# Optimization experiments

Hardware: AMD Instinct MI355X
Metric: run time of the kernel (lower is better)

Reference implementation:

```python
import jax, jax.numpy as jnp
import numpy as np

HIDDEN = 1024
HEADS = 16
D_HEAD = HIDDEN // HEADS  # 64
N = 2048


def setup_inputs() -> dict:
    key = jax.random.key(0)
    ks = jax.random.split(key, 12)
    s = 1.0 / np.sqrt(HIDDEN)
    return {
        "q": jax.random.normal(ks[0], (N, HIDDEN), jnp.float32),
        "k": jax.random.normal(ks[1], (N, HIDDEN), jnp.float32),
        "v": jax.random.normal(ks[2], (N, HIDDEN), jnp.float32),
        "attn_bias": jax.random.normal(ks[3], (HEADS, 1, N, N), jnp.float32),
        "Wq": jax.random.normal(ks[4], (HIDDEN, HIDDEN), jnp.float32) * s,
        "bq": jax.random.normal(ks[5], (HIDDEN,), jnp.float32) * s,
        "Wk": jax.random.normal(ks[6], (HIDDEN, HIDDEN), jnp.float32) * s,
        "bk": jax.random.normal(ks[7], (HIDDEN,), jnp.float32) * s,
        "Wv": jax.random.normal(ks[8], (HIDDEN, HIDDEN), jnp.float32) * s,
        "bv": jax.random.normal(ks[9], (HIDDEN,), jnp.float32) * s,
        "Wo": jax.random.normal(ks[10], (HIDDEN, HIDDEN), jnp.float32) * s,
        "bo": jax.random.normal(ks[11], (HIDDEN,), jnp.float32) * s,
    }


def reference(q, k, v, attn_bias, Wq, bq, Wk, bk, Wv, bv, Wo, bo):
    # q,k,v: [N, hidden]; attn_bias: [H, 1, N, N]. Attention runs over the
    # node axis (dim 0 in the torch code), inner seq dim is 1 (squeezed).
    n = q.shape[0]
    scale = D_HEAD ** -0.5
    qh = (q @ Wq.T + bq).reshape(n, HEADS, D_HEAD).transpose(1, 0, 2)  # [H,N,d]
    kh = (k @ Wk.T + bk).reshape(n, HEADS, D_HEAD).transpose(1, 0, 2)  # [H,N,d]
    vh = (v @ Wv.T + bv).reshape(n, HEADS, D_HEAD).transpose(1, 0, 2)  # [H,N,d]
    scores = jnp.einsum('hnd,hmd->hnm', qh * scale, kh) + attn_bias[:, 0]  # [H,N,N]
    attn = jax.nn.softmax(scores, axis=-1)
    ctx = jnp.einsum('hnm,hmd->hnd', attn, vh)            # [H,N,d]
    ctx = ctx.transpose(1, 0, 2).reshape(n, HEADS * D_HEAD)  # [N,hidden]
    return ctx @ Wo.T + bo
```

## Files before the change

kernel.cpp:

```cpp
#include <hip/hip_runtime.h>
#include <type_traits>
#include <utility>

#define NT 2048
#define HD 1024
#define NHEAD 16
#define DHEAD 64
#define LOG2E 1.44269504f

typedef float f32x4 __attribute__((ext_vector_type(4)));
typedef __bf16 b16x8 __attribute__((ext_vector_type(8)));
typedef short s16x8 __attribute__((ext_vector_type(8)));
typedef unsigned short u16x8 __attribute__((ext_vector_type(8)));
typedef unsigned short u16x4 __attribute__((ext_vector_type(4)));

template <typename V, typename = void>
struct mfma_takes : std::false_type {};
template <typename V>
struct mfma_takes<V, std::void_t<decltype(__builtin_amdgcn_mfma_f32_16x16x32_bf16(
                         std::declval<V>(), std::declval<V>(), std::declval<f32x4>(), 0, 0, 0))>>
    : std::true_type {};

template <typename V>
__device__ __forceinline__ f32x4 mfma_impl(V a, V b, f32x4 c) {
  return __builtin_amdgcn_mfma_f32_16x16x32_bf16(a, b, c, 0, 0, 0);
}

__device__ __forceinline__ f32x4 mfma_bf16(u16x8 a, u16x8 b, f32x4 c) {
  using V = typename std::conditional<mfma_takes<b16x8>::value, b16x8, s16x8>::type;
  return mfma_impl<V>(__builtin_bit_cast(V, a), __builtin_bit_cast(V, b), c);
}

__device__ __forceinline__ unsigned short f2bf(float f) {
  unsigned int u = __builtin_bit_cast(unsigned int, f);
  return (unsigned short)((u + 0x7FFFu + ((u >> 16) & 1u)) >> 16);
}

__device__ __forceinline__ void gload16(const unsigned short* g, unsigned short* l) {
  __builtin_amdgcn_global_load_lds(
      (__attribute__((address_space(1))) void*)(void*)(g),
      (__attribute__((address_space(3))) void*)(void*)(l), 16, 0, 0);
}

__device__ __forceinline__ void barrier_pinned() {
  __builtin_amdgcn_sched_barrier(0);
  __builtin_amdgcn_s_barrier();
  __builtin_amdgcn_sched_barrier(0);
}
#define WAIT_VM6() asm volatile("s_waitcnt vmcnt(6)" ::: "memory")
#define WAIT_VM0() asm volatile("s_waitcnt vmcnt(0)" ::: "memory")
#define WAIT_LGKM0() asm volatile("s_waitcnt lgkmcnt(0)" ::: "memory")

__global__ __launch_bounds__(256) void cvt_bf16(
    const float* __restrict__ s0, const float* __restrict__ s1, const float* __restrict__ s2,
    const float* __restrict__ s3, const float* __restrict__ s4, const float* __restrict__ s5,
    const float* __restrict__ s6,
    unsigned short* __restrict__ d0, unsigned short* __restrict__ d1, unsigned short* __restrict__ d2,
    unsigned short* __restrict__ d3, unsigned short* __restrict__ d4, unsigned short* __restrict__ d5,
    unsigned short* __restrict__ d6) {
  const int seg = blockIdx.y;
  const float* s;
  unsigned short* d;
  switch (seg) {
    case 0: s = s0; d = d0; break;
    case 1: s = s1; d = d1; break;
    case 2: s = s2; d = d2; break;
    case 3: s = s3; d = d3; break;
    case 4: s = s4; d = d4; break;
    case 5: s = s5; d = d5; break;
    default: s = s6; d = d6; break;
  }
  const int n = (seg < 3) ? NT * HD : HD * HD;
  for (int i = blockIdx.x * 2048 + threadIdx.x * 8; i < n; i += gridDim.x * 2048) {
    f32x4 f0 = *reinterpret_cast<const f32x4*>(&s[i]);
    f32x4 f1 = *reinterpret_cast<const f32x4*>(&s[i + 4]);
    u16x8 o;
#pragma unroll
    for (int e = 0; e < 4; ++e) { o[e] = f2bf(f0[e]); o[e + 4] = f2bf(f1[e]); }
    *reinterpret_cast<u16x8*>(&d[i]) = o;
  }
}

__device__ __forceinline__ void gemm64x128(
    const unsigned short* __restrict__ A, const unsigned short* __restrict__ B,
    int n0, int m0,
    unsigned short* As0, unsigned short* As1,
    unsigned short* Bs0, unsigned short* Bs1, f32x4 acc[2][4]) {
  const int tid = threadIdx.x;
  const int lane = tid & 63;
  const int wr = (tid >> 6) >> 1, wc = (tid >> 6) & 1;
  const int srow = tid >> 3;
  const int scol = (((tid & 7) ^ (srow & 7)) << 3);

  auto stage = [&](int kt, unsigned short* as, unsigned short* bs) {
#pragma unroll
    for (int p = 0; p < 2; ++p)
      gload16(&A[(size_t)(n0 + p * 32 + srow) * HD + kt + scol], as + p * 2048 + tid * 8);
#pragma unroll
    for (int p = 0; p < 4; ++p)
      gload16(&B[(size_t)(m0 + p * 32 + srow) * HD + kt + scol], bs + p * 2048 + tid * 8);
  };
  auto comp = [&](const unsigned short* as, const unsigned short* bs) {
#pragma unroll
    for (int ks = 0; ks < 2; ++ks) {
      const int q = ks * 4 + (lane >> 4);
      u16x8 a[2], b[4];
#pragma unroll
      for (int i = 0; i < 2; ++i) {
        const int row = wr * 32 + i * 16 + (lane & 15);
        a[i] = *reinterpret_cast<const u16x8*>(&as[row * 64 + ((q ^ (row & 7)) << 3)]);
      }
#pragma unroll
      for (int j = 0; j < 4; ++j) {
        const int row = wc * 64 + j * 16 + (lane & 15);
        b[j] = *reinterpret_cast<const u16x8*>(&bs[row * 64 + ((q ^ (row & 7)) << 3)]);
      }
#pragma unroll
      for (int i = 0; i < 2; ++i)
#pragma unroll
        for (int j = 0; j < 4; ++j)
          acc[i][j] = mfma_bf16(a[i], b[j], acc[i][j]);
    }
  };

  stage(0, As0, Bs0);
  stage(64, As1, Bs1);
#pragma unroll 1
  for (int s = 0; s < 14; ++s) {
    WAIT_VM6();
    barrier_pinned();
    if (s & 1) comp(As1, Bs1); else comp(As0, Bs0);
    barrier_pinned();
    if (s & 1) stage((s + 2) * 64, As1, Bs1);
    else       stage((s + 2) * 64, As0, Bs0);
  }
  WAIT_VM6();
  barrier_pinned();
  comp(As0, Bs0);
  WAIT_VM0();
  barrier_pinned();
  comp(As1, Bs1);
}

__global__ __launch_bounds__(256) void proj_gemm(
    const unsigned short* __restrict__ qb, const unsigned short* __restrict__ kb,
    const unsigned short* __restrict__ vb,
    const unsigned short* __restrict__ Wqb, const unsigned short* __restrict__ Wkb,
    const unsigned short* __restrict__ Wvb,
    const float* __restrict__ bq, const float* __restrict__ bk, const float* __restrict__ bv,
    unsigned short* __restrict__ Qh, unsigned short* __restrict__ Kh,
    unsigned short* __restrict__ Vt) {
  const int L = blockIdx.x;
  const int m = L / 96;
  const int c = L % 96;
  const int z = c / 32;
  const int n = c % 32;
  const int n0 = n * 64, m0 = m * 128;

  const unsigned short* A = (z == 0) ? qb : (z == 1) ? kb : vb;
  const unsigned short* B = (z == 0) ? Wqb : (z == 1) ? Wkb : Wvb;
  const float* bias = (z == 0) ? bq : (z == 1) ? bk : bv;

  __shared__ unsigned short As0[64 * 64], As1[64 * 64];
  __shared__ unsigned short Bs0[128 * 64], Bs1[128 * 64];

  const int tid = threadIdx.x;
  const int lane = tid & 63;
  const int wr = (tid >> 6) >> 1, wc = (tid >> 6) & 1;

  f32x4 acc[2][4] = {};
  gemm64x128(A, B, n0, m0, As0, As1, Bs0, Bs1, acc);

  const int rgrp = (lane >> 4) * 4;
  const float scale = (z == 0) ? 0.125f * LOG2E : 1.0f;
#pragma unroll
  for (int i = 0; i < 2; ++i) {
    const int nb = n0 + wr * 32 + i * 16 + rgrp;
#pragma unroll
    for (int j = 0; j < 4; ++j) {
      const int mcol = m0 + wc * 64 + j * 16 + (lane & 15);
      const float bb = bias[mcol];
      if (z == 2) {
        u16x4 pk;
#pragma unroll
        for (int r = 0; r < 4; ++r) pk[r] = f2bf(acc[i][j][r] + bb);
        *reinterpret_cast<u16x4*>(&Vt[(size_t)mcol * NT + nb]) = pk;
      } else {
        unsigned short* dst = (z == 0) ? Qh : Kh;
#pragma unroll
        for (int r = 0; r < 4; ++r)
          dst[(size_t)(nb + r) * HD + mcol] = f2bf((acc[i][j][r] + bb) * scale);
      }
    }
  }
}

__global__ __launch_bounds__(256, 2) void attn_kernel(
    const unsigned short* __restrict__ Qh, const unsigned short* __restrict__ Kh,
    const unsigned short* __restrict__ Vt, const float* __restrict__ bias,
    unsigned short* __restrict__ ctx) {
  const int id = blockIdx.x;
  const int xcd = id & 7, slot = id >> 3;
  const int h = xcd * 2 + (slot >> 5);
  const int q0 = (slot & 31) * 64;
  const int tid = threadIdx.x;
  const int lane = tid & 63;
  const int wave = tid >> 6;

  __shared__ unsigned short Ks0[128 * 64], Ks1[128 * 64];
  __shared__ unsigned short Vs0[64 * 128], Vs1[64 * 128];
  __shared__ unsigned short Ps[4 * 16 * 128];

  u16x8 qf[2];
  {
    const int qrow = q0 + wave * 16 + (lane & 15);
    const int db = (lane >> 4) * 8;
    qf[0] = *reinterpret_cast<const u16x8*>(&Qh[(size_t)qrow * HD + h * DHEAD + db]);
    qf[1] = *reinterpret_cast<const u16x8*>(&Qh[(size_t)qrow * HD + h * DHEAD + 32 + db]);
  }

  f32x4 oacc[4] = {};
  float mrun[4], lrun[4];
#pragma unroll
  for (int r = 0; r < 4; ++r) { mrun[r] = -3.0e38f; lrun[r] = 0.f; }

  const float* bias_h = bias + (size_t)h * NT * NT;
  const int qlrow = q0 + wave * 16 + (lane >> 4) * 4;
  const float* bias_l = bias_h + (size_t)qlrow * NT + (lane & 15);

  const unsigned short* Kbase = Kh + h * DHEAD;
  const unsigned short* Vbase = Vt + (size_t)h * DHEAD * NT;

  const int krow = tid >> 3;
  const int kchk = tid & 7;
  const int vrow = tid >> 4;
  const int vchk = tid & 15;

  auto stage = [&](int t, unsigned short* ks, unsigned short* vs) {
    const int kt = t * 128;
#pragma unroll
    for (int p = 0; p < 4; ++p) {
      const int r = p * 32 + krow;
      gload16(&Kbase[(size_t)(kt + r) * HD + ((kchk ^ (r & 7)) << 3)], ks + p * 2048 + tid * 8);
    }
#pragma unroll
    for (int p = 0; p < 4; ++p) {
      const int r = p * 16 + vrow;
      gload16(&Vbase[(size_t)r * NT + kt + ((vchk ^ (r & 7)) << 3)], vs + p * 2048 + tid * 8);
    }
  };

  float br[8][4];
#pragma unroll
  for (int j = 0; j < 8; ++j)
#pragma unroll
    for (int r = 0; r < 4; ++r) br[j][r] = bias_l[(size_t)r * NT + j * 16];
  stage(0, Ks0, Vs0);
  WAIT_VM0();
  barrier_pinned();

  unsigned short* const psw = Ps + wave * 2048;

#pragma unroll 1
  for (int t = 0; t < NT / 128; ++t) {
    const bool more = (t + 1 < NT / 128);
    const unsigned short* ks = (t & 1) ? Ks1 : Ks0;
    const unsigned short* vs = (t & 1) ? Vs1 : Vs0;

    if (more) stage(t + 1, (t & 1) ? Ks0 : Ks1, (t & 1) ? Vs0 : Vs1);

    f32x4 s[8] = {};
#pragma unroll
    for (int kss = 0; kss < 2; ++kss) {
      const int q = kss * 4 + (lane >> 4);
#pragma unroll
      for (int j = 0; j < 8; ++j) {
        const int row = j * 16 + (lane & 15);
        u16x8 kf = *reinterpret_cast<const u16x8*>(&ks[row * 64 + ((q ^ (row & 7)) << 3)]);
        s[j] = mfma_bf16(qf[kss], kf, s[j]);
      }
    }
#pragma unroll
    for (int j = 0; j < 8; ++j)
#pragma unroll
      for (int r = 0; r < 4; ++r) s[j][r] = fmaf(br[j][r], LOG2E, s[j][r]);

    if (more) {
      const float* bp = bias_l + (size_t)(t + 1) * 128;
#pragma unroll
      for (int j = 0; j < 8; ++j)
#pragma unroll
        for (int r = 0; r < 4; ++r) br[j][r] = bp[(size_t)r * NT + j * 16];
    }

    float mnew[4];
#pragma unroll
    for (int r = 0; r < 4; ++r) {
      float mx = s[0][r];
#pragma unroll
      for (int j = 1; j < 8; ++j) mx = fmaxf(mx, s[j][r]);
      mx = fmaxf(mx, __shfl_xor(mx, 1));
      mx = fmaxf(mx, __shfl_xor(mx, 2));
      mx = fmaxf(mx, __shfl_xor(mx, 4));
      mx = fmaxf(mx, __shfl_xor(mx, 8));
      mnew[r] = fmaxf(mrun[r], mx);
    }
#pragma unroll
    for (int r = 0; r < 4; ++r) {
      const float corr = exp2f(mrun[r] - mnew[r]);
      lrun[r] *= corr;
#pragma unroll
      for (int nd = 0; nd < 4; ++nd) oacc[nd][r] *= corr;
      mrun[r] = mnew[r];
    }
    float psum[4] = {0.f, 0.f, 0.f, 0.f};
#pragma unroll
    for (int j = 0; j < 8; ++j) {
      const int chkbase = j * 2 + ((lane >> 3) & 1);
      const int cofs = lane & 7;
#pragma unroll
      for (int r = 0; r < 4; ++r) {
        const int row = (lane >> 4) * 4 + r;
        const float p = exp2f(s[j][r] - mrun[r]);
        psum[r] += p;
        psw[row * 128 + ((chkbase ^ (row & 7)) << 3) + cofs] = f2bf(p);
      }
    }
#pragma unroll
    for (int r = 0; r < 4; ++r) {
      float tsum = psum[r];
      tsum += __shfl_xor(tsum, 1);
      tsum += __shfl_xor(tsum, 2);
      tsum += __shfl_xor(tsum, 4);
      tsum += __shfl_xor(tsum, 8);
      lrun[r] += tsum;
    }

#pragma unroll
    for (int kk = 0; kk < 4; ++kk) {
      const int q = kk * 4 + (lane >> 4);
      const int prow = lane & 15;
      u16x8 pa = *reinterpret_cast<const u16x8*>(&psw[prow * 128 + ((q ^ (prow & 7)) << 3)]);
#pragma unroll
      for (int nd = 0; nd < 4; ++nd) {
        const int vr = nd * 16 + (lane & 15);
        u16x8 vb = *reinterpret_cast<const u16x8*>(&vs[vr * 128 + ((q ^ (vr & 7)) << 3)]);
        oacc[nd] = mfma_bf16(pa, vb, oacc[nd]);
      }
    }

    WAIT_VM0();
    barrier_pinned();
  }

#pragma unroll
  for (int nd = 0; nd < 4; ++nd) {
#pragma unroll
    for (int r = 0; r < 4; ++r) {
      const float val = oacc[nd][r] / lrun[r];
      ctx[(size_t)(qlrow + r) * HD + h * DHEAD + nd * 16 + (lane & 15)] = f2bf(val);
    }
  }
}

__global__ __launch_bounds__(256) void out_gemm(
    const unsigned short* __restrict__ Ain, const unsigned short* __restrict__ Wob,
    const float* __restrict__ bias, float* __restrict__ out) {
  const int L = blockIdx.x;
  const int m = L / 32;
  const int n = L % 32;
  const int n0 = n * 64, m0 = m * 128;

  __shared__ unsigned short As0[64 * 64], As1[64 * 64];
  __shared__ unsigned short Bs0[128 * 64], Bs1[128 * 64];

  const int tid = threadIdx.x;
  const int lane = tid & 63;
  const int wr = (tid >> 6) >> 1, wc = (tid >> 6) & 1;

  f32x4 acc[2][4] = {};
  gemm64x128(Ain, Wob, n0, m0, As0, As1, Bs0, Bs1, acc);

  const int rgrp = (lane >> 4) * 4;
#pragma unroll
  for (int i = 0; i < 2; ++i) {
    const int nb = n0 + wr * 32 + i * 16 + rgrp;
#pragma unroll
    for (int j = 0; j < 4; ++j) {
      const int mcol = m0 + wc * 64 + j * 16 + (lane & 15);
      const float bb = bias[mcol];
#pragma unroll
      for (int r = 0; r < 4; ++r)
        out[(size_t)(nb + r) * HD + mcol] = acc[i][j][r] + bb;
    }
  }
}

extern "C" void kernel_launch(void* const* d_in, const int* in_sizes, int n_in,
                              void* d_out, int out_size, void* d_ws, size_t ws_size,
                              hipStream_t stream) {
  const float* q  = (const float*)d_in[0];
  const float* k  = (const float*)d_in[1];
  const float* v  = (const float*)d_in[2];
  const float* ab = (const float*)d_in[3];
  const float* Wq = (const float*)d_in[4];
  const float* bq = (const float*)d_in[5];
  const float* Wk = (const float*)d_in[6];
  const float* bk = (const float*)d_in[7];
  const float* Wv = (const float*)d_in[8];
  const float* bv = (const float*)d_in[9];
  const float* Wo = (const float*)d_in[10];
  const float* bo = (const float*)d_in[11];

  unsigned short* qb  = (unsigned short*)d_ws;
  unsigned short* kb  = qb + (size_t)NT * HD;
  unsigned short* vb  = kb + (size_t)NT * HD;
  unsigned short* Wqb = vb + (size_t)NT * HD;
  unsigned short* Wkb = Wqb + (size_t)HD * HD;
  unsigned short* Wvb = Wkb + (size_t)HD * HD;
  unsigned short* Wob = Wvb + (size_t)HD * HD;
  unsigned short* Qh  = Wob + (size_t)HD * HD;
  unsigned short* Kh  = Qh + (size_t)NT * HD;
  unsigned short* Vt  = Kh + (size_t)NT * HD;
  unsigned short* ctx = Vt + (size_t)NT * HD;

  cvt_bf16<<<dim3(512, 7), 256, 0, stream>>>(q, k, v, Wq, Wk, Wv, Wo,
                                             qb, kb, vb, Wqb, Wkb, Wvb, Wob);
  proj_gemm<<<dim3(768), 256, 0, stream>>>(
      qb, kb, vb, Wqb, Wkb, Wvb, bq, bk, bv, Qh, Kh, Vt);
  attn_kernel<<<dim3(512), 256, 0, stream>>>(Qh, Kh, Vt, ab, ctx);
  out_gemm<<<dim3(256), 256, 0, stream>>>(ctx, Wob, bo, (float*)d_out);
}
```

Measured before the change: 119.3 us.

## Fuse fp32-to-bf16 activation conversion into projection GEMM; shrink out_gemm tile

The projection GEMM now reads q/k/v in fp32 through registers, converts them to bf16 and writes them to shared memory inside its pipelined k-loop. The separate conversion pass over the activations and its bf16 workspace round trip go away, and only the weights are still pre-converted. The output GEMM switches from 64x128 to 64x64 tiles, doubling its grid to 512 blocks for better CU occupancy. The trade-off is more VGPR pressure and extra register-staged work in the projection loop, plus twice the A-tile reloads in the output GEMM.

```diff
diff --git a/kernel.cpp b/kernel.cpp
--- a/kernel.cpp
+++ b/kernel.cpp
@@ -47,17 +47,16 @@
   __builtin_amdgcn_s_barrier();
   __builtin_amdgcn_sched_barrier(0);
 }
-#define WAIT_VM6() asm volatile("s_waitcnt vmcnt(6)" ::: "memory")
+#define WAIT_VM8() asm volatile("s_waitcnt vmcnt(8)" ::: "memory")
+#define WAIT_VM4() asm volatile("s_waitcnt vmcnt(4)" ::: "memory")
 #define WAIT_VM0() asm volatile("s_waitcnt vmcnt(0)" ::: "memory")
 #define WAIT_LGKM0() asm volatile("s_waitcnt lgkmcnt(0)" ::: "memory")
 
 __global__ __launch_bounds__(256) void cvt_bf16(
     const float* __restrict__ s0, const float* __restrict__ s1, const float* __restrict__ s2,
-    const float* __restrict__ s3, const float* __restrict__ s4, const float* __restrict__ s5,
-    const float* __restrict__ s6,
-    unsigned short* __restrict__ d0, unsigned short* __restrict__ d1, unsigned short* __restrict__ d2,
-    unsigned short* __restrict__ d3, unsigned short* __restrict__ d4, unsigned short* __restrict__ d5,
-    unsigned short* __restrict__ d6) {
+    const float* __restrict__ s3,
+    unsigned short* __restrict__ d0, unsigned short* __restrict__ d1,
+    unsigned short* __restrict__ d2, unsigned short* __restrict__ d3) {
   const int seg = blockIdx.y;
   const float* s;
   unsigned short* d;
@@ -65,86 +64,20 @@
     case 0: s = s0; d = d0; break;
     case 1: s = s1; d = d1; break;
     case 2: s = s2; d = d2; break;
-    case 3: s = s3; d = d3; break;
-    case 4: s = s4; d = d4; break;
-    case 5: s = s5; d = d5; break;
-    default: s = s6; d = d6; break;
-  }
-  const int n = (seg < 3) ? NT * HD : HD * HD;
-  for (int i = blockIdx.x * 2048 + threadIdx.x * 8; i < n; i += gridDim.x * 2048) {
-    f32x4 f0 = *reinterpret_cast<const f32x4*>(&s[i]);
-    f32x4 f1 = *reinterpret_cast<const f32x4*>(&s[i + 4]);
-    u16x8 o;
-#pragma unroll
-    for (int e = 0; e < 4; ++e) { o[e] = f2bf(f0[e]); o[e + 4] = f2bf(f1[e]); }
-    *reinterpret_cast<u16x8*>(&d[i]) = o;
-  }
-}
-
-__device__ __forceinline__ void gemm64x128(
-    const unsigned short* __restrict__ A, const unsigned short* __restrict__ B,
-    int n0, int m0,
-    unsigned short* As0, unsigned short* As1,
-    unsigned short* Bs0, unsigned short* Bs1, f32x4 acc[2][4]) {
-  const int tid = threadIdx.x;
-  const int lane = tid & 63;
-  const int wr = (tid >> 6) >> 1, wc = (tid >> 6) & 1;
-  const int srow = tid >> 3;
-  const int scol = (((tid & 7) ^ (srow & 7)) << 3);
-
-  auto stage = [&](int kt, unsigned short* as, unsigned short* bs) {
-#pragma unroll
-    for (int p = 0; p < 2; ++p)
-      gload16(&A[(size_t)(n0 + p * 32 + srow) * HD + kt + scol], as + p * 2048 + tid * 8);
-#pragma unroll
-    for (int p = 0; p < 4; ++p)
-      gload16(&B[(size_t)(m0 + p * 32 + srow) * HD + kt + scol], bs + p * 2048 + tid * 8);
-  };
-  auto comp = [&](const unsigned short* as, const unsigned short* bs) {
-#pragma unroll
-    for (int ks = 0; ks < 2; ++ks) {
-      const int q = ks * 4 + (lane >> 4);
-      u16x8 a[2], b[4];
-#pragma unroll
-      for (int i = 0; i < 2; ++i) {
-        const int row = wr * 32 + i * 16 + (lane & 15);
-        a[i] = *reinterpret_cast<const u16x8*>(&as[row * 64 + ((q ^ (row & 7)) << 3)]);
-      }
-#pragma unroll
-      for (int j = 0; j < 4; ++j) {
-        const int row = wc * 64 + j * 16 + (lane & 15);
-        b[j] = *reinterpret_cast<const u16x8*>(&bs[row * 64 + ((q ^ (row & 7)) << 3)]);
-      }
-#pragma unroll
-      for (int i = 0; i < 2; ++i)
-#pragma unroll
-        for (int j = 0; j < 4; ++j)
-          acc[i][j] = mfma_bf16(a[i], b[j], acc[i][j]);
-    }
-  };
-
-  stage(0, As0, Bs0);
-  stage(64, As1, Bs1);
-#pragma unroll 1
-  for (int s = 0; s < 14; ++s) {
-    WAIT_VM6();
-    barrier_pinned();
-    if (s & 1) comp(As1, Bs1); else comp(As0, Bs0);
-    barrier_pinned();
-    if (s & 1) stage((s + 2) * 64, As1, Bs1);
-    else       stage((s + 2) * 64, As0, Bs0);
-  }
-  WAIT_VM6();
-  barrier_pinned();
-  comp(As0, Bs0);
-  WAIT_VM0();
-  barrier_pinned();
-  comp(As1, Bs1);
+    default: s = s3; d = d3; break;
+  }
+  const int i = blockIdx.x * 2048 + threadIdx.x * 8;
+  f32x4 f0 = *reinterpret_cast<const f32x4*>(&s[i]);
+  f32x4 f1 = *reinterpret_cast<const f32x4*>(&s[i + 4]);
+  u16x8 o;
+#pragma unroll
+  for (int e = 0; e < 4; ++e) { o[e] = f2bf(f0[e]); o[e + 4] = f2bf(f1[e]); }
+  *reinterpret_cast<u16x8*>(&d[i]) = o;
 }
 
 __global__ __launch_bounds__(256) void proj_gemm(
-    const unsigned short* __restrict__ qb, const unsigned short* __restrict__ kb,
-    const unsigned short* __restrict__ vb,
+    const float* __restrict__ qf32, const float* __restrict__ kf32,
+    const float* __restrict__ vf32,
     const unsigned short* __restrict__ Wqb, const unsigned short* __restrict__ Wkb,
     const unsigned short* __restrict__ Wvb,
     const float* __restrict__ bq, const float* __restrict__ bk, const float* __restrict__ bv,
@@ -157,7 +90,7 @@
   const int n = c % 32;
   const int n0 = n * 64, m0 = m * 128;
 
-  const unsigned short* A = (z == 0) ? qb : (z == 1) ? kb : vb;
+  const float* A = (z == 0) ? qf32 : (z == 1) ? kf32 : vf32;
   const unsigned short* B = (z == 0) ? Wqb : (z == 1) ? Wkb : Wvb;
   const float* bias = (z == 0) ? bq : (z == 1) ? bk : bv;
 
@@ -167,9 +100,91 @@
   const int tid = threadIdx.x;
   const int lane = tid & 63;
   const int wr = (tid >> 6) >> 1, wc = (tid >> 6) & 1;
-
+  const int srow = tid >> 3;
+  const int schk = (tid & 7) ^ (srow & 7);
+  const int scol = schk << 3;
+
+  f32x4 areg[4];
+
+  auto issueA = [&](int kt) {
+#pragma unroll
+    for (int p = 0; p < 2; ++p) {
+      const float* src = &A[(size_t)(n0 + p * 32 + srow) * HD + kt + scol];
+      areg[p * 2 + 0] = *reinterpret_cast<const f32x4*>(src);
+      areg[p * 2 + 1] = *reinterpret_cast<const f32x4*>(src + 4);
+    }
+  };
+  auto finishA = [&](unsigned short* as) {
+#pragma unroll
+    for (int p = 0; p < 2; ++p) {
+      u16x8 o;
+#pragma unroll
+      for (int e = 0; e < 4; ++e) {
+        o[e] = f2bf(areg[p * 2 + 0][e]);
+        o[e + 4] = f2bf(areg[p * 2 + 1][e]);
+      }
+      *reinterpret_cast<u16x8*>(&as[p * 2048 + tid * 8]) = o;
+    }
+  };
+  auto issueB = [&](int kt, unsigned short* bs) {
+#pragma unroll
+    for (int p = 0; p < 4; ++p)
+      gload16(&B[(size_t)(m0 + p * 32 + srow) * HD + kt + scol], bs + p * 2048 + tid * 8);
+  };
   f32x4 acc[2][4] = {};
-  gemm64x128(A, B, n0, m0, As0, As1, Bs0, Bs1, acc);
+  auto comp = [&](const unsigned short* as, const unsigned short* bs) {
+#pragma unroll
+    for (int ks = 0; ks < 2; ++ks) {
+      const int q = ks * 4 + (lane >> 4);
+      u16x8 a[2], b[4];
+#pragma unroll
+      for (int i = 0; i < 2; ++i) {
+        const int row = wr * 32 + i * 16 + (lane & 15);
+        a[i] = *reinterpret_cast<const u16x8*>(&as[row * 64 + ((q ^ (row & 7)) << 3)]);
+      }
+#pragma unroll
+      for (int j = 0; j < 4; ++j) {
+        const int row = wc * 64 + j * 16 + (lane & 15);
+        b[j] = *reinterpret_cast<const u16x8*>(&bs[row * 64 + ((q ^ (row & 7)) << 3)]);
+      }
+#pragma unroll
+      for (int i = 0; i < 2; ++i)
+#pragma unroll
+        for (int j = 0; j < 4; ++j)
+          acc[i][j] = mfma_bf16(a[i], b[j], acc[i][j]);
+    }
+  };
+
+  issueA(0);
+  issueB(0, Bs0);
+  WAIT_VM4();
+  finishA(As0);
+  issueA(64);
+  issueB(64, Bs1);
+
+#pragma unroll 1
+  for (int s = 0; s < 14; ++s) {
+    WAIT_VM8();
+    WAIT_LGKM0();
+    barrier_pinned();
+    if (s & 1) comp(As1, Bs1); else comp(As0, Bs0);
+    barrier_pinned();
+    WAIT_VM4();
+    finishA((s & 1) ? As0 : As1);
+    issueA((s + 2) * 64);
+    issueB((s + 2) * 64, (s & 1) ? Bs1 : Bs0);
+  }
+  WAIT_VM8();
+  WAIT_LGKM0();
+  barrier_pinned();
+  comp(As0, Bs0);
+  barrier_pinned();
+  WAIT_VM4();
+  finishA(As1);
+  WAIT_VM0();
+  WAIT_LGKM0();
+  barrier_pinned();
+  comp(As1, Bs1);
 
   const int rgrp = (lane >> 4) * 4;
   const float scale = (z == 0) ? 0.125f * LOG2E : 1.0f;
@@ -369,25 +384,74 @@
   const int L = blockIdx.x;
   const int m = L / 32;
   const int n = L % 32;
-  const int n0 = n * 64, m0 = m * 128;
+  const int n0 = n * 64, m0 = m * 64;
 
   __shared__ unsigned short As0[64 * 64], As1[64 * 64];
-  __shared__ unsigned short Bs0[128 * 64], Bs1[128 * 64];
+  __shared__ unsigned short Bs0[64 * 64], Bs1[64 * 64];
 
   const int tid = threadIdx.x;
   const int lane = tid & 63;
   const int wr = (tid >> 6) >> 1, wc = (tid >> 6) & 1;
-
-  f32x4 acc[2][4] = {};
-  gemm64x128(Ain, Wob, n0, m0, As0, As1, Bs0, Bs1, acc);
+  const int srow = tid >> 3;
+  const int scol = (((tid & 7) ^ (srow & 7)) << 3);
+
+  auto stage = [&](int kt, unsigned short* as, unsigned short* bs) {
+#pragma unroll
+    for (int p = 0; p < 2; ++p)
+      gload16(&Ain[(size_t)(n0 + p * 32 + srow) * HD + kt + scol], as + p * 2048 + tid * 8);
+#pragma unroll
+    for (int p = 0; p < 2; ++p)
+      gload16(&Wob[(size_t)(m0 + p * 32 + srow) * HD + kt + scol], bs + p * 2048 + tid * 8);
+  };
+  f32x4 acc[2][2] = {};
+  auto comp = [&](const unsigned short* as, const unsigned short* bs) {
+#pragma unroll
+    for (int ks = 0; ks < 2; ++ks) {
+      const int q = ks * 4 + (lane >> 4);
+      u16x8 a[2], b[2];
+#pragma unroll
+      for (int i = 0; i < 2; ++i) {
+        const int row = wr * 32 + i * 16 + (lane & 15);
+        a[i] = *reinterpret_cast<const u16x8*>(&as[row * 64 + ((q ^ (row & 7)) << 3)]);
+      }
+#pragma unroll
+      for (int j = 0; j < 2; ++j) {
+        const int row = wc * 32 + j * 16 + (lane & 15);
+        b[j] = *reinterpret_cast<const u16x8*>(&bs[row * 64 + ((q ^ (row & 7)) << 3)]);
+      }
+#pragma unroll
+      for (int i = 0; i < 2; ++i)
+#pragma unroll
+        for (int j = 0; j < 2; ++j)
+          acc[i][j] = mfma_bf16(a[i], b[j], acc[i][j]);
+    }
+  };
+
+  stage(0, As0, Bs0);
+  stage(64, As1, Bs1);
+#pragma unroll 1
+  for (int s = 0; s < 14; ++s) {
+    WAIT_VM4();
+    barrier_pinned();
+    if (s & 1) comp(As1, Bs1); else comp(As0, Bs0);
+    barrier_pinned();
+    if (s & 1) stage((s + 2) * 64, As1, Bs1);
+    else       stage((s + 2) * 64, As0, Bs0);
+  }
+  WAIT_VM4();
+  barrier_pinned();
+  comp(As0, Bs0);
+  WAIT_VM0();
+  barrier_pinned();
+  comp(As1, Bs1);
 
   const int rgrp = (lane >> 4) * 4;
 #pragma unroll
   for (int i = 0; i < 2; ++i) {
     const int nb = n0 + wr * 32 + i * 16 + rgrp;
 #pragma unroll
-    for (int j = 0; j < 4; ++j) {
-      const int mcol = m0 + wc * 64 + j * 16 + (lane & 15);
+    for (int j = 0; j < 2; ++j) {
+      const int mcol = m0 + wc * 32 + j * 16 + (lane & 15);
       const float bb = bias[mcol];
 #pragma unroll
       for (int r = 0; r < 4; ++r)
@@ -412,10 +476,7 @@
   const float* Wo = (const float*)d_in[10];
   const float* bo = (const float*)d_in[11];
 
-  unsigned short* qb  = (unsigned short*)d_ws;
-  unsigned short* kb  = qb + (size_t)NT * HD;
-  unsigned short* vb  = kb + (size_t)NT * HD;
-  unsigned short* Wqb = vb + (size_t)NT * HD;
+  unsigned short* Wqb = (unsigned short*)d_ws;
   unsigned short* Wkb = Wqb + (size_t)HD * HD;
   unsigned short* Wvb = Wkb + (size_t)HD * HD;
   unsigned short* Wob = Wvb + (size_t)HD * HD;
@@ -424,10 +485,9 @@
   unsigned short* Vt  = Kh + (size_t)NT * HD;
   unsigned short* ctx = Vt + (size_t)NT * HD;
 
-  cvt_bf16<<<dim3(512, 7), 256, 0, stream>>>(q, k, v, Wq, Wk, Wv, Wo,
-                                             qb, kb, vb, Wqb, Wkb, Wvb, Wob);
+  cvt_bf16<<<dim3(512, 4), 256, 0, stream>>>(Wq, Wk, Wv, Wo, Wqb, Wkb, Wvb, Wob);
   proj_gemm<<<dim3(768), 256, 0, stream>>>(
-      qb, kb, vb, Wqb, Wkb, Wvb, bq, bk, bv, Qh, Kh, Vt);
+      q, k, v, Wqb, Wkb, Wvb, bq, bk, bv, Qh, Kh, Vt);
   attn_kernel<<<dim3(512), 256, 0, stream>>>(Qh, Kh, Vt, ab, ctx);
-  out_gemm<<<dim3(256), 256, 0, stream>>>(ctx, Wob, bo, (float*)d_out);
-}
+  out_gemm<<<dim3(512), 256, 0, stream>>>(ctx, Wob, bo, (float*)d_out);
+}
```

Result: no change. 120.4 us (+0.9%).

## Shrink output GEMM tile to 64x64 for more blocks; relax attention loop wait

Applied to the files above, without the earlier changes.

The output projection GEMM switches from 64x128 tiles over 256 blocks to 64x64 tiles over 512 blocks. It gets its own double-buffered global-to-LDS pipeline with a vmcnt(4) wait, so more of the GPU's compute units get work. In the attention kernel, the end-of-iteration wait changes from vmcnt(0) to vmcnt(32), so outstanding loads can overlap the barrier. The relaxed wait risks reading LDS before loads land if the count does not match the issued loads, and smaller tiles lower per-block data reuse.

```diff
diff --git a/kernel.cpp b/kernel.cpp
--- a/kernel.cpp
+++ b/kernel.cpp
@@ -47,7 +47,9 @@
   __builtin_amdgcn_s_barrier();
   __builtin_amdgcn_sched_barrier(0);
 }
+#define WAIT_VM32() asm volatile("s_waitcnt vmcnt(32)" ::: "memory")
 #define WAIT_VM6() asm volatile("s_waitcnt vmcnt(6)" ::: "memory")
+#define WAIT_VM4() asm volatile("s_waitcnt vmcnt(4)" ::: "memory")
 #define WAIT_VM0() asm volatile("s_waitcnt vmcnt(0)" ::: "memory")
 #define WAIT_LGKM0() asm volatile("s_waitcnt lgkmcnt(0)" ::: "memory")
 
@@ -349,7 +351,7 @@
       }
     }
 
-    WAIT_VM0();
+    WAIT_VM32();
     barrier_pinned();
   }
 
@@ -369,25 +371,74 @@
   const int L = blockIdx.x;
   const int m = L / 32;
   const int n = L % 32;
-  const int n0 = n * 64, m0 = m * 128;
+  const int n0 = n * 64, m0 = m * 64;
 
   __shared__ unsigned short As0[64 * 64], As1[64 * 64];
-  __shared__ unsigned short Bs0[128 * 64], Bs1[128 * 64];
+  __shared__ unsigned short Bs0[64 * 64], Bs1[64 * 64];
 
   const int tid = threadIdx.x;
   const int lane = tid & 63;
   const int wr = (tid >> 6) >> 1, wc = (tid >> 6) & 1;
-
-  f32x4 acc[2][4] = {};
-  gemm64x128(Ain, Wob, n0, m0, As0, As1, Bs0, Bs1, acc);
+  const int srow = tid >> 3;
+  const int scol = (((tid & 7) ^ (srow & 7)) << 3);
+
+  auto stage = [&](int kt, unsigned short* as, unsigned short* bs) {
+#pragma unroll
+    for (int p = 0; p < 2; ++p)
+      gload16(&Ain[(size_t)(n0 + p * 32 + srow) * HD + kt + scol], as + p * 2048 + tid * 8);
+#pragma unroll
+    for (int p = 0; p < 2; ++p)
+      gload16(&Wob[(size_t)(m0 + p * 32 + srow) * HD + kt + scol], bs + p * 2048 + tid * 8);
+  };
+  f32x4 acc[2][2] = {};
+  auto comp = [&](const unsigned short* as, const unsigned short* bs) {
+#pragma unroll
+    for (int ks = 0; ks < 2; ++ks) {
+      const int q = ks * 4 + (lane >> 4);
+      u16x8 a[2], b[2];
+#pragma unroll
+      for (int i = 0; i < 2; ++i) {
+        const int row = wr * 32 + i * 16 + (lane & 15);
+        a[i] = *reinterpret_cast<const u16x8*>(&as[row * 64 + ((q ^ (row & 7)) << 3)]);
+      }
+#pragma unroll
+      for (int j = 0; j < 2; ++j) {
+        const int row = wc * 32 + j * 16 + (lane & 15);
+        b[j] = *reinterpret_cast<const u16x8*>(&bs[row * 64 + ((q ^ (row & 7)) << 3)]);
+      }
+#pragma unroll
+      for (int i = 0; i < 2; ++i)
+#pragma unroll
+        for (int j = 0; j < 2; ++j)
+          acc[i][j] = mfma_bf16(a[i], b[j], acc[i][j]);
+    }
+  };
+
+  stage(0, As0, Bs0);
+  stage(64, As1, Bs1);
+#pragma unroll 1
+  for (int s = 0; s < 14; ++s) {
+    WAIT_VM4();
+    barrier_pinned();
+    if (s & 1) comp(As1, Bs1); else comp(As0, Bs0);
+    barrier_pinned();
+    if (s & 1) stage((s + 2) * 64, As1, Bs1);
+    else       stage((s + 2) * 64, As0, Bs0);
+  }
+  WAIT_VM4();
+  barrier_pinned();
+  comp(As0, Bs0);
+  WAIT_VM0();
+  barrier_pinned();
+  comp(As1, Bs1);
 
   const int rgrp = (lane >> 4) * 4;
 #pragma unroll
   for (int i = 0; i < 2; ++i) {
     const int nb = n0 + wr * 32 + i * 16 + rgrp;
 #pragma unroll
-    for (int j = 0; j < 4; ++j) {
-      const int mcol = m0 + wc * 64 + j * 16 + (lane & 15);
+    for (int j = 0; j < 2; ++j) {
+      const int mcol = m0 + wc * 32 + j * 16 + (lane & 15);
       const float bb = bias[mcol];
 #pragma unroll
       for (int r = 0; r < 4; ++r)
@@ -429,5 +480,5 @@
   proj_gemm<<<dim3(768), 256, 0, stream>>>(
       qb, kb, vb, Wqb, Wkb, Wvb, bq, bk, bv, Qh, Kh, Vt);
   attn_kernel<<<dim3(512), 256, 0, stream>>>(Qh, Kh, Vt, ab, ctx);
-  out_gemm<<<dim3(256), 256, 0, stream>>>(ctx, Wob, bo, (float*)d_out);
-}
+  out_gemm<<<dim3(512), 256, 0, stream>>>(ctx, Wob, bo, (float*)d_out);
+}
```

Result: no change. 118.3 us, median of 2 (-0.8%).
